# Optimization experiments

Hardware: AMD Instinct MI355X
Metric: run time of the kernel (lower is better)

Reference implementation:

```python
import jax, jax.numpy as jnp
import numpy as np

N_NODES = 100000
D_FEAT = 128
N_EDGES = 1600000


def setup_inputs() -> dict:
    key = jax.random.key(0)
    k1, k2, k3 = jax.random.split(key, 3)
    x = jax.random.normal(k1, (N_NODES, D_FEAT), dtype=jnp.float32)
    edge_weight = jax.random.uniform(k2, (N_EDGES,), dtype=jnp.float32)
    edge_index = jax.random.randint(k3, (2, N_EDGES), 0, N_NODES, dtype=jnp.int64)
    return {"x": x, "edge_weight": edge_weight, "edge_index": edge_index, "n_nodes": N_NODES}


def reference(x, edge_weight, edge_index, n_nodes):
    # h_v = sum_{(u->v) in E} w_uv * h_u  (gather -> scale -> scatter_add)
    src = edge_index[0]
    dst = edge_index[1]
    msg = x[src] * edge_weight[:, None]          # (E, d)
    out = jax.ops.segment_sum(msg, dst, num_segments=n_nodes)  # (N, d)
    return out
```

## Files before the change

### kernel.cpp

```cpp
#include <hip/hip_runtime.h>
#include <math.h>


constexpr int D_FEAT = 128;
constexpr int NPB = 128;
constexpr int LOG_NPB = 7;
constexpr int NBK_MAX = 1024;
constexpr int SCB = 128;
constexpr int CAP = 3072;

typedef float v4f __attribute__((ext_vector_type(4)));

__global__ __launch_bounds__(256) void scatter_atomic_kernel(
    const float* __restrict__ x, const float* __restrict__ w,
    const int* __restrict__ src_idx, const int* __restrict__ dst_idx,
    float* __restrict__ out, int n_edges) {
  long long tid = (long long)blockIdx.x * blockDim.x + threadIdx.x;
  int lane = (int)(tid & 31);
  long long e = tid >> 5;
  if (e >= n_edges) return;
  int s = src_idx[e];
  int d = dst_idx[e];
  float wt = w[e];
  float4 v = ((const float4*)(x + (size_t)s * D_FEAT))[lane];
  float* o = out + (size_t)d * D_FEAT + (size_t)lane * 4;
  atomicAdd(o + 0, v.x * wt);
  atomicAdd(o + 1, v.y * wt);
  atomicAdd(o + 2, v.z * wt);
  atomicAdd(o + 3, v.w * wt);
}

__device__ __forceinline__ int block_excl_scan(int v, int* sh, int* total) {
  const int lane = threadIdx.x & 63;
  const int wid = threadIdx.x >> 6;
  const int nw = blockDim.x >> 6;
  int inc = v;
  #pragma unroll
  for (int o = 1; o < 64; o <<= 1) {
    int t = __shfl_up(inc, o, 64);
    if (lane >= o) inc += t;
  }
  if (lane == 63) sh[wid] = inc;
  __syncthreads();
  if (threadIdx.x == 0) {
    int a = 0;
    for (int k = 0; k < nw; ++k) { int t = sh[k]; sh[k] = a; a += t; }
    sh[nw] = a;
  }
  __syncthreads();
  int r = sh[wid] + inc - v;
  if (total) *total = sh[nw];
  __syncthreads();
  return r;
}

__global__ __launch_bounds__(512) void hist_kernel(
    const int* __restrict__ dst, int* __restrict__ gtot,
    int* __restrict__ gcur, int* __restrict__ gbase, int* __restrict__ done,
    int n_edges, int nbk, int tile, int pad8) {
  __shared__ int h[NBK_MAX];
  __shared__ int sh[9];
  __shared__ int slast;
  const int tid = threadIdx.x;
  const int b = blockIdx.x;
  for (int k = tid; k < nbk; k += 512) h[k] = 0;
  __syncthreads();
  int base = b * tile;
  int lim = min(base + tile, n_edges);
  for (int i = base + tid; i < lim; i += 512)
    atomicAdd(&h[((unsigned)dst[i]) >> LOG_NPB], 1);
  __syncthreads();
  for (int k = tid; k < nbk; k += 512) {
    int v = h[k];
    if (v) {
      int r = pad8 ? ((v + 7) & ~7) : v;
      atomicAdd(&gtot[k], r);
    }
  }
  __threadfence();
  __syncthreads();
  if (tid == 0)
    slast = (__hip_atomic_fetch_add(done, 1, __ATOMIC_ACQ_REL,
                                    __HIP_MEMORY_SCOPE_AGENT) ==
             (int)gridDim.x - 1);
  __syncthreads();
  if (slast) {
    int carry = 0;
    for (int kb = 0; kb < nbk; kb += 512) {
      int k = kb + tid;
      int v = (k < nbk)
                  ? __hip_atomic_load(&gtot[k], __ATOMIC_RELAXED,
                                      __HIP_MEMORY_SCOPE_AGENT)
                  : 0;
      int tot;
      int ex = block_excl_scan(v, sh, &tot);
      if (k < nbk) { gbase[k] = carry + ex; gcur[k] = carry + ex; }
      carry += tot;
    }
    if (tid == 0) gbase[nbk] = carry;
  }
}

__global__ __launch_bounds__(256) void init_seg_kernel(int* __restrict__ gcur,
                                                       int nbk, int capb) {
  int k = blockIdx.x * 256 + threadIdx.x;
  if (k < nbk) gcur[k] = k * capb;
}

__global__ __launch_bounds__(512) void scatter_kernel(
    const int* __restrict__ src, const int* __restrict__ dst,
    const float* __restrict__ w, int* __restrict__ gcur,
    uint2* __restrict__ csr, int n_edges, int nbk, int tile, int capb,
    int pad8) {
  __shared__ int h[NBK_MAX];
  __shared__ int cur[NBK_MAX];
  __shared__ int gb[NBK_MAX];
  const int tid = threadIdx.x;
  const int b = blockIdx.x;
  int base = b * tile;
  int lim = min(base + tile, n_edges);
  for (int k = tid; k < nbk; k += 512) h[k] = 0;
  __syncthreads();
  for (int i = base + tid; i < lim; i += 512)
    atomicAdd(&h[((unsigned)dst[i]) >> LOG_NPB], 1);
  __syncthreads();
  for (int k = tid; k < nbk; k += 512) {
    cur[k] = 0;
    int v = h[k];
    if (v) {
      int r = pad8 ? ((v + 7) & ~7) : v;
      int g = atomicAdd(&gcur[k], r);
      if (capb && (g + r > (k + 1) * capb)) g = -1;
      gb[k] = g;
      if (g >= 0) {
        for (int p = v; p < r; ++p)
          csr[g + p] =
              make_uint2(((unsigned)(g + p) & (NPB - 1u)) << 20, 0u);
      }
    } else {
      gb[k] = -1;
    }
  }
  __syncthreads();
  for (int i = base + tid; i < lim; i += 512) {
    unsigned d = (unsigned)dst[i];
    unsigned k = d >> LOG_NPB;
    int pos = atomicAdd(&cur[k], 1);
    int g = gb[k];
    if (g >= 0)
      csr[g + pos] = make_uint2((unsigned)src[i] | ((d & (NPB - 1u)) << 20),
                                __float_as_uint(w[i]));
  }
}

__global__ __launch_bounds__(256) void gather_kernel(
    const float* __restrict__ x, const int* __restrict__ gbase,
    const int* __restrict__ gcur, const uint2* __restrict__ csr,
    float* __restrict__ out, int n_nodes, int capb,
    const int* __restrict__ src, const int* __restrict__ dst,
    const float* __restrict__ w, int n_edges) {
  __shared__ uint2 eds[CAP];
  __shared__ unsigned short perm[CAP];
  __shared__ int loff[NPB + 1];
  __shared__ int lcur[NPB];
  __shared__ int sh[9];

  const int b = blockIdx.x;
  const int tid = threadIdx.x;
  const int beg = capb ? b * capb : gbase[b];
  const int cnt = gcur[b] - beg;
  const int limcap = capb ? capb : CAP;
  const int nbase = b * NPB;

  const int wv = tid >> 6;
  const int lane = tid & 63;
  const int f = lane & 31;
  const int half = lane >> 5;
  const float4* X = (const float4*)x;

  if (cnt <= limcap) {
    if (tid < NPB) lcur[tid] = 0;
    __syncthreads();
    for (int i = tid; i < cnt; i += 256) {
      uint2 e = csr[beg + i];
      eds[i] = e;
      atomicAdd(&lcur[e.x >> 20], 1);
    }
    __syncthreads();
    {
      int v = (tid < NPB) ? lcur[tid] : 0;
      int ex = block_excl_scan(v, sh, nullptr);
      __syncthreads();
      if (tid < NPB) { loff[tid] = ex; lcur[tid] = 0; }
      if (tid == 0) loff[NPB] = cnt;
    }
    __syncthreads();
    for (int i = tid; i < cnt; i += 256) {
      int dl = eds[i].x >> 20;
      int pos = loff[dl] + atomicAdd(&lcur[dl], 1);
      perm[pos] = (unsigned short)i;
    }
    __syncthreads();

    for (int n = wv; n < NPB; n += 4) {
      int node = nbase + n;
      if (node >= n_nodes) break;
      int jb = loff[n];
      int je = loff[n + 1];
      float4 a0 = make_float4(0.f, 0.f, 0.f, 0.f);
      float4 a1 = make_float4(0.f, 0.f, 0.f, 0.f);
      float4 a2 = make_float4(0.f, 0.f, 0.f, 0.f);
      float4 a3 = make_float4(0.f, 0.f, 0.f, 0.f);
      int j = jb + half;
      for (; j + 6 < je; j += 8) {
        uint2 e0 = eds[perm[j]];
        uint2 e1 = eds[perm[j + 2]];
        uint2 e2 = eds[perm[j + 4]];
        uint2 e3 = eds[perm[j + 6]];
        float4 v0 = X[(size_t)(e0.x & 0xFFFFFu) * 32 + f];
        float4 v1 = X[(size_t)(e1.x & 0xFFFFFu) * 32 + f];
        float4 v2 = X[(size_t)(e2.x & 0xFFFFFu) * 32 + f];
        float4 v3 = X[(size_t)(e3.x & 0xFFFFFu) * 32 + f];
        float w0 = __uint_as_float(e0.y);
        float w1 = __uint_as_float(e1.y);
        float w2 = __uint_as_float(e2.y);
        float w3 = __uint_as_float(e3.y);
        a0.x += w0 * v0.x; a0.y += w0 * v0.y; a0.z += w0 * v0.z; a0.w += w0 * v0.w;
        a1.x += w1 * v1.x; a1.y += w1 * v1.y; a1.z += w1 * v1.z; a1.w += w1 * v1.w;
        a2.x += w2 * v2.x; a2.y += w2 * v2.y; a2.z += w2 * v2.z; a2.w += w2 * v2.w;
        a3.x += w3 * v3.x; a3.y += w3 * v3.y; a3.z += w3 * v3.z; a3.w += w3 * v3.w;
      }
      for (; j < je; j += 2) {
        uint2 e0 = eds[perm[j]];
        float4 v0 = X[(size_t)(e0.x & 0xFFFFFu) * 32 + f];
        float w0 = __uint_as_float(e0.y);
        a0.x += w0 * v0.x; a0.y += w0 * v0.y; a0.z += w0 * v0.z; a0.w += w0 * v0.w;
      }
      a0.x += a1.x + a2.x + a3.x;
      a0.y += a1.y + a2.y + a3.y;
      a0.z += a1.z + a2.z + a3.z;
      a0.w += a1.w + a2.w + a3.w;
      a0.x += __shfl_xor(a0.x, 32, 64);
      a0.y += __shfl_xor(a0.y, 32, 64);
      a0.z += __shfl_xor(a0.z, 32, 64);
      a0.w += __shfl_xor(a0.w, 32, 64);
      if (half == 0) {
        v4f val = {a0.x, a0.y, a0.z, a0.w};
        __builtin_nontemporal_store(val, (v4f*)out + (size_t)node * 32 + f);
      }
    }
  } else {
    for (int n = wv; n < NPB; n += 4) {
      int node = nbase + n;
      if (node >= n_nodes) break;
      float4 a0 = make_float4(0.f, 0.f, 0.f, 0.f);
      for (int j = half; j < n_edges; j += 2) {
        if (dst[j] == node) {
          float4 v = X[(size_t)src[j] * 32 + f];
          float wt = w[j];
          a0.x += wt * v.x; a0.y += wt * v.y; a0.z += wt * v.z; a0.w += wt * v.w;
        }
      }
      a0.x += __shfl_xor(a0.x, 32, 64);
      a0.y += __shfl_xor(a0.y, 32, 64);
      a0.z += __shfl_xor(a0.z, 32, 64);
      a0.w += __shfl_xor(a0.w, 32, 64);
      if (half == 0) {
        v4f val = {a0.x, a0.y, a0.z, a0.w};
        __builtin_nontemporal_store(val, (v4f*)out + (size_t)node * 32 + f);
      }
    }
  }
}

extern "C" void kernel_launch(void* const* d_in, const int* in_sizes, int n_in,
                              void* d_out, int out_size, void* d_ws, size_t ws_size,
                              hipStream_t stream) {
  const float* x  = (const float*)d_in[0];
  const float* w  = (const float*)d_in[1];
  const int* eidx = (const int*)d_in[2];

  int n_edges = in_sizes[1];
  int n_nodes = out_size / D_FEAT;
  const int* src = eidx;
  const int* dst = eidx + n_edges;
  float* out = (float*)d_out;

  if (n_edges <= 0) {
    hipMemsetAsync(d_out, 0, (size_t)out_size * sizeof(float), stream);
    return;
  }

  const int nbk = (n_nodes + NPB - 1) / NPB;
  const int stile = (n_edges + SCB - 1) / SCB;

  const size_t ctrl_ints = (size_t)NBK_MAX + NBK_MAX + 4 + (NBK_MAX + 4);
  const size_t ctrl_bytes = ctrl_ints * 4;
  long long slots_avail = ((long long)ws_size - (long long)ctrl_bytes) / 8;

  long long mean = n_edges / (nbk > 0 ? nbk : 1);
  int capb_min = (int)(mean + 7.0 * sqrt((double)(mean > 0 ? mean : 1)) +
                       3.5 * SCB + 8.0 * sqrt((double)SCB) + 16);
  int capb = 0;
  if (nbk > 0 && slots_avail > 0) {
    long long c = slots_avail / nbk;
    if (c > CAP) c = CAP;
    capb = (int)(c & ~7LL);
  }
  long long worst_pad = (long long)SCB * nbk * 7;
  bool seg_ok = (capb >= capb_min && capb_min <= CAP);
  bool exact_pad_ok = (slots_avail >= (long long)n_edges + worst_pad + 16);
  bool exact_ok = (slots_avail >= (long long)n_edges);

  if ((!seg_ok && !exact_ok) || nbk > NBK_MAX || n_nodes >= (1 << 20)) {
    hipMemsetAsync(d_out, 0, (size_t)out_size * sizeof(float), stream);
    long long total_threads = (long long)n_edges * 32;
    long long grid = (total_threads + 255) / 256;
    scatter_atomic_kernel<<<(dim3)(unsigned)grid, 256, 0, stream>>>(
        x, w, src, dst, out, n_edges);
    return;
  }

  int* gtot = (int*)d_ws;
  int* gcur = gtot + NBK_MAX;
  int* done = gcur + NBK_MAX;
  int* gbase = done + 4;
  uint2* csr = (uint2*)(gbase + NBK_MAX + 4);

  if (seg_ok) {
    init_seg_kernel<<<(nbk + 255) / 256, 256, 0, stream>>>(gcur, nbk, capb);
    scatter_kernel<<<SCB, 512, 0, stream>>>(src, dst, w, gcur, csr,
                                            n_edges, nbk, stile, capb, 1);
    gather_kernel<<<nbk, 256, 0, stream>>>(x, gbase, gcur, csr, out, n_nodes,
                                           capb, src, dst, w, n_edges);
  } else {
    int pad8 = exact_pad_ok ? 1 : 0;
    hipMemsetAsync(gtot, 0, (size_t)(NBK_MAX * 2 + 4) * sizeof(int), stream);
    hist_kernel<<<SCB, 512, 0, stream>>>(dst, gtot, gcur, gbase, done,
                                         n_edges, nbk, stile, pad8);
    scatter_kernel<<<SCB, 512, 0, stream>>>(src, dst, w, gcur, csr,
                                            n_edges, nbk, stile, 0, pad8);
    gather_kernel<<<nbk, 256, 0, stream>>>(x, gbase, gcur, csr, out, n_nodes,
                                           0, src, dst, w, n_edges);
  }
}
```

Measured before the change: 262.8 us.

## Fuse bucket init, scatter and gather into one cooperative grid-synced kernel

Replaces the init/scatter/gather kernel sequence with a single cooperative kernel of nbk blocks that uses grid.sync between phases. Each block bins its edge tile into per-bucket CSR segments, then locally sorts its bucket's edges by destination in shared memory and accumulates rows without atomics. Padding-to-8 is dropped and the capacity bound is loosened. This removes launch gaps and raises scatter parallelism from 128 to 782 blocks. The cost is two grid-wide barriers, a cooperative launch that needs all 782 blocks co-resident (about 25KB LDS each), and a slow fallback path.

```diff
diff --git a/kernel.cpp b/kernel.cpp
--- a/kernel.cpp
+++ b/kernel.cpp
@@ -1,12 +1,15 @@
 #include <hip/hip_runtime.h>
+#include <hip/hip_cooperative_groups.h>
 #include <math.h>
+
+namespace cg = cooperative_groups;
 
 
 constexpr int D_FEAT = 128;
 constexpr int NPB = 128;
 constexpr int LOG_NPB = 7;
 constexpr int NBK_MAX = 1024;
-constexpr int SCB = 128;
+constexpr int SCB = 256;
 constexpr int CAP = 3072;
 
 typedef float v4f __attribute__((ext_vector_type(4)));
@@ -54,10 +57,168 @@
   return r;
 }
 
+__global__ __launch_bounds__(256) void fused_kernel(
+    const float* __restrict__ x, const float* __restrict__ w,
+    const int* __restrict__ src, const int* __restrict__ dst,
+    int* __restrict__ gcur, uint2* __restrict__ csr,
+    float* __restrict__ out, int n_edges, int n_nodes, int nbk, int tile,
+    int capb) {
+  __shared__ union SM {
+    struct { int h[NBK_MAX]; int cur[NBK_MAX]; int gb[NBK_MAX]; } sc;
+    struct {
+      uint2 eds[CAP];
+      unsigned short perm[CAP];
+      int loff[NPB + 1];
+      int lcur[NPB];
+      int sh[9];
+    } ga;
+  } sm;
+  cg::grid_group grid = cg::this_grid();
+  const int tid = threadIdx.x;
+  const int b = blockIdx.x;
+
+  if (tid == 0) gcur[b] = b * capb;
+  for (int k = tid; k < nbk; k += 256) sm.sc.h[k] = 0;
+  __syncthreads();
+  grid.sync();
+
+  int base = b * tile;
+  int lim = min(base + tile, n_edges);
+  for (int i = base + tid; i < lim; i += 256)
+    atomicAdd(&sm.sc.h[((unsigned)dst[i]) >> LOG_NPB], 1);
+  __syncthreads();
+  for (int k = tid; k < nbk; k += 256) {
+    sm.sc.cur[k] = 0;
+    int v = sm.sc.h[k];
+    int g = -1;
+    if (v) {
+      g = atomicAdd(&gcur[k], v);
+      if (g + v > (k + 1) * capb) g = -1;
+    }
+    sm.sc.gb[k] = g;
+  }
+  __syncthreads();
+  for (int i = base + tid; i < lim; i += 256) {
+    unsigned d = (unsigned)dst[i];
+    unsigned k = d >> LOG_NPB;
+    int pos = atomicAdd(&sm.sc.cur[k], 1);
+    int g = sm.sc.gb[k];
+    if (g >= 0)
+      csr[g + pos] = make_uint2((unsigned)src[i] | ((d & (NPB - 1u)) << 20),
+                                __float_as_uint(w[i]));
+  }
+  __threadfence();
+  grid.sync();
+
+  const int beg = b * capb;
+  const int cnt = gcur[b] - beg;
+  const int nbase = b * NPB;
+  const int wv = tid >> 6;
+  const int lane = tid & 63;
+  const int f = lane & 31;
+  const int half = lane >> 5;
+  const float4* X = (const float4*)x;
+
+  if (cnt <= capb) {
+    if (tid < NPB) sm.ga.lcur[tid] = 0;
+    __syncthreads();
+    for (int i = tid; i < cnt; i += 256) {
+      uint2 e = csr[beg + i];
+      sm.ga.eds[i] = e;
+      atomicAdd(&sm.ga.lcur[e.x >> 20], 1);
+    }
+    __syncthreads();
+    {
+      int v = (tid < NPB) ? sm.ga.lcur[tid] : 0;
+      int ex = block_excl_scan(v, sm.ga.sh, nullptr);
+      __syncthreads();
+      if (tid < NPB) { sm.ga.loff[tid] = ex; sm.ga.lcur[tid] = 0; }
+      if (tid == 0) sm.ga.loff[NPB] = cnt;
+    }
+    __syncthreads();
+    for (int i = tid; i < cnt; i += 256) {
+      int dl = sm.ga.eds[i].x >> 20;
+      int pos = sm.ga.loff[dl] + atomicAdd(&sm.ga.lcur[dl], 1);
+      sm.ga.perm[pos] = (unsigned short)i;
+    }
+    __syncthreads();
+
+    for (int n = wv; n < NPB; n += 4) {
+      int node = nbase + n;
+      if (node >= n_nodes) break;
+      int jb = sm.ga.loff[n];
+      int je = sm.ga.loff[n + 1];
+      float4 a0 = make_float4(0.f, 0.f, 0.f, 0.f);
+      float4 a1 = make_float4(0.f, 0.f, 0.f, 0.f);
+      float4 a2 = make_float4(0.f, 0.f, 0.f, 0.f);
+      float4 a3 = make_float4(0.f, 0.f, 0.f, 0.f);
+      int j = jb + half;
+      for (; j + 6 < je; j += 8) {
+        uint2 e0 = sm.ga.eds[sm.ga.perm[j]];
+        uint2 e1 = sm.ga.eds[sm.ga.perm[j + 2]];
+        uint2 e2 = sm.ga.eds[sm.ga.perm[j + 4]];
+        uint2 e3 = sm.ga.eds[sm.ga.perm[j + 6]];
+        float4 v0 = X[(size_t)(e0.x & 0xFFFFFu) * 32 + f];
+        float4 v1 = X[(size_t)(e1.x & 0xFFFFFu) * 32 + f];
+        float4 v2 = X[(size_t)(e2.x & 0xFFFFFu) * 32 + f];
+        float4 v3 = X[(size_t)(e3.x & 0xFFFFFu) * 32 + f];
+        float w0 = __uint_as_float(e0.y);
+        float w1 = __uint_as_float(e1.y);
+        float w2 = __uint_as_float(e2.y);
+        float w3 = __uint_as_float(e3.y);
+        a0.x += w0 * v0.x; a0.y += w0 * v0.y; a0.z += w0 * v0.z; a0.w += w0 * v0.w;
+        a1.x += w1 * v1.x; a1.y += w1 * v1.y; a1.z += w1 * v1.z; a1.w += w1 * v1.w;
+        a2.x += w2 * v2.x; a2.y += w2 * v2.y; a2.z += w2 * v2.z; a2.w += w2 * v2.w;
+        a3.x += w3 * v3.x; a3.y += w3 * v3.y; a3.z += w3 * v3.z; a3.w += w3 * v3.w;
+      }
+      for (; j < je; j += 2) {
+        uint2 e0 = sm.ga.eds[sm.ga.perm[j]];
+        float4 v0 = X[(size_t)(e0.x & 0xFFFFFu) * 32 + f];
+        float w0 = __uint_as_float(e0.y);
+        a0.x += w0 * v0.x; a0.y += w0 * v0.y; a0.z += w0 * v0.z; a0.w += w0 * v0.w;
+      }
+      a0.x += a1.x + a2.x + a3.x;
+      a0.y += a1.y + a2.y + a3.y;
+      a0.z += a1.z + a2.z + a3.z;
+      a0.w += a1.w + a2.w + a3.w;
+      a0.x += __shfl_xor(a0.x, 32, 64);
+      a0.y += __shfl_xor(a0.y, 32, 64);
+      a0.z += __shfl_xor(a0.z, 32, 64);
+      a0.w += __shfl_xor(a0.w, 32, 64);
+      if (half == 0) {
+        v4f val = {a0.x, a0.y, a0.z, a0.w};
+        __builtin_nontemporal_store(val, (v4f*)out + (size_t)node * 32 + f);
+      }
+    }
+  } else {
+    for (int n = wv; n < NPB; n += 4) {
+      int node = nbase + n;
+      if (node >= n_nodes) break;
+      float4 a0 = make_float4(0.f, 0.f, 0.f, 0.f);
+      for (int j = half; j < n_edges; j += 2) {
+        if (dst[j] == node) {
+          float4 v = X[(size_t)src[j] * 32 + f];
+          float wt = w[j];
+          a0.x += wt * v.x; a0.y += wt * v.y; a0.z += wt * v.z; a0.w += wt * v.w;
+        }
+      }
+      a0.x += __shfl_xor(a0.x, 32, 64);
+      a0.y += __shfl_xor(a0.y, 32, 64);
+      a0.z += __shfl_xor(a0.z, 32, 64);
+      a0.w += __shfl_xor(a0.w, 32, 64);
+      if (half == 0) {
+        v4f val = {a0.x, a0.y, a0.z, a0.w};
+        __builtin_nontemporal_store(val, (v4f*)out + (size_t)node * 32 + f);
+      }
+    }
+  }
+}
+
+
 __global__ __launch_bounds__(512) void hist_kernel(
     const int* __restrict__ dst, int* __restrict__ gtot,
     int* __restrict__ gcur, int* __restrict__ gbase, int* __restrict__ done,
-    int n_edges, int nbk, int tile, int pad8) {
+    int n_edges, int nbk, int tile) {
   __shared__ int h[NBK_MAX];
   __shared__ int sh[9];
   __shared__ int slast;
@@ -70,13 +231,8 @@
   for (int i = base + tid; i < lim; i += 512)
     atomicAdd(&h[((unsigned)dst[i]) >> LOG_NPB], 1);
   __syncthreads();
-  for (int k = tid; k < nbk; k += 512) {
-    int v = h[k];
-    if (v) {
-      int r = pad8 ? ((v + 7) & ~7) : v;
-      atomicAdd(&gtot[k], r);
-    }
-  }
+  for (int k = tid; k < nbk; k += 512)
+    if (h[k]) atomicAdd(&gtot[k], h[k]);
   __threadfence();
   __syncthreads();
   if (tid == 0)
@@ -110,8 +266,7 @@
 __global__ __launch_bounds__(512) void scatter_kernel(
     const int* __restrict__ src, const int* __restrict__ dst,
     const float* __restrict__ w, int* __restrict__ gcur,
-    uint2* __restrict__ csr, int n_edges, int nbk, int tile, int capb,
-    int pad8) {
+    uint2* __restrict__ csr, int n_edges, int nbk, int tile, int capb) {
   __shared__ int h[NBK_MAX];
   __shared__ int cur[NBK_MAX];
   __shared__ int gb[NBK_MAX];
@@ -127,19 +282,12 @@
   for (int k = tid; k < nbk; k += 512) {
     cur[k] = 0;
     int v = h[k];
+    int g = -1;
     if (v) {
-      int r = pad8 ? ((v + 7) & ~7) : v;
-      int g = atomicAdd(&gcur[k], r);
-      if (capb && (g + r > (k + 1) * capb)) g = -1;
-      gb[k] = g;
-      if (g >= 0) {
-        for (int p = v; p < r; ++p)
-          csr[g + p] =
-              make_uint2(((unsigned)(g + p) & (NPB - 1u)) << 20, 0u);
-      }
-    } else {
-      gb[k] = -1;
-    }
+      g = atomicAdd(&gcur[k], v);
+      if (capb && (g + v > (k + 1) * capb)) g = -1;
+    }
+    gb[k] = g;
   }
   __syncthreads();
   for (int i = base + tid; i < lim; i += 512) {
@@ -292,6 +440,7 @@
   }
 
   const int nbk = (n_nodes + NPB - 1) / NPB;
+  const int ftile = (n_edges + nbk - 1) / nbk;
   const int stile = (n_edges + SCB - 1) / SCB;
 
   const size_t ctrl_ints = (size_t)NBK_MAX + NBK_MAX + 4 + (NBK_MAX + 4);
@@ -299,17 +448,14 @@
   long long slots_avail = ((long long)ws_size - (long long)ctrl_bytes) / 8;
 
   long long mean = n_edges / (nbk > 0 ? nbk : 1);
-  int capb_min = (int)(mean + 7.0 * sqrt((double)(mean > 0 ? mean : 1)) +
-                       3.5 * SCB + 8.0 * sqrt((double)SCB) + 16);
+  int capb_min = (int)(mean + 7.0 * sqrt((double)(mean > 0 ? mean : 1)) + 32);
   int capb = 0;
   if (nbk > 0 && slots_avail > 0) {
     long long c = slots_avail / nbk;
     if (c > CAP) c = CAP;
     capb = (int)(c & ~7LL);
   }
-  long long worst_pad = (long long)SCB * nbk * 7;
   bool seg_ok = (capb >= capb_min && capb_min <= CAP);
-  bool exact_pad_ok = (slots_avail >= (long long)n_edges + worst_pad + 16);
   bool exact_ok = (slots_avail >= (long long)n_edges);
 
   if ((!seg_ok && !exact_ok) || nbk > NBK_MAX || n_nodes >= (1 << 20)) {
@@ -328,18 +474,24 @@
   uint2* csr = (uint2*)(gbase + NBK_MAX + 4);
 
   if (seg_ok) {
+    int fe = n_edges, fn = n_nodes, fb = nbk, ft = ftile, fc = capb;
+    void* kargs[] = {(void*)&x,    (void*)&w,   (void*)&src, (void*)&dst,
+                     (void*)&gcur, (void*)&csr, (void*)&out, (void*)&fe,
+                     (void*)&fn,   (void*)&fb,  (void*)&ft,  (void*)&fc};
+    hipError_t err = hipLaunchCooperativeKernel(
+        (void*)fused_kernel, dim3((unsigned)nbk), dim3(256), kargs, 0, stream);
+    if (err == hipSuccess) return;
     init_seg_kernel<<<(nbk + 255) / 256, 256, 0, stream>>>(gcur, nbk, capb);
     scatter_kernel<<<SCB, 512, 0, stream>>>(src, dst, w, gcur, csr,
-                                            n_edges, nbk, stile, capb, 1);
+                                            n_edges, nbk, stile, capb);
     gather_kernel<<<nbk, 256, 0, stream>>>(x, gbase, gcur, csr, out, n_nodes,
                                            capb, src, dst, w, n_edges);
   } else {
-    int pad8 = exact_pad_ok ? 1 : 0;
     hipMemsetAsync(gtot, 0, (size_t)(NBK_MAX * 2 + 4) * sizeof(int), stream);
     hist_kernel<<<SCB, 512, 0, stream>>>(dst, gtot, gcur, gbase, done,
-                                         n_edges, nbk, stile, pad8);
+                                         n_edges, nbk, stile);
     scatter_kernel<<<SCB, 512, 0, stream>>>(src, dst, w, gcur, csr,
-                                            n_edges, nbk, stile, 0, pad8);
+                                            n_edges, nbk, stile, 0);
     gather_kernel<<<nbk, 256, 0, stream>>>(x, gbase, gcur, csr, out, n_nodes,
                                            0, src, dst, w, n_edges);
   }
```

Measured after the change: 497.6 us. 1.89x slower.
